# Performance work log

Hardware: AMD Instinct MI355X
Metric: run time of the kernel (lower is better)

Reference implementation:

```python
import jax, jax.numpy as jnp
import numpy as np

N = 50000
H = 8
D = 32
E = 400000
IN = 128
NEG_SLOPE = 0.2


def _gat(h, edges, W, al, ar, b):
    # DGL GATConv: fc -> per-head attention logits -> edge softmax over dst -> aggregate
    src, dst = edges[0], edges[1]
    feat = (h @ W).reshape(N, H, D)                      # [N,H,D]
    el = jnp.einsum('nhd,hd->nh', feat, al)              # [N,H]
    er = jnp.einsum('nhd,hd->nh', feat, ar)              # [N,H]
    e = jax.nn.leaky_relu(el[src] + er[dst], NEG_SLOPE)  # [E,H]
    m = jax.ops.segment_max(e, dst, num_segments=N)      # [N,H] per-dst max
    m = jnp.where(jnp.isfinite(m), m, 0.0)
    m = jax.lax.stop_gradient(m)
    ex = jnp.exp(e - m[dst])                             # [E,H]
    denom = jax.ops.segment_sum(ex, dst, num_segments=N) # [N,H]
    alpha = ex / denom[dst]                              # edge softmax
    out = jax.ops.segment_sum(feat[src] * alpha[:, :, None], dst, num_segments=N)  # [N,H,D]
    return (out + b.reshape(1, H, D)).reshape(N, H * D)


def setup_inputs() -> dict:
    key = jax.random.key(0)
    ks = jax.random.split(key, 12)
    s = 0.05
    return {
        'h': jax.random.normal(ks[0], (N, IN), jnp.float32),
        'edges0': jax.random.randint(ks[1], (2, E), 0, N, jnp.int32),
        'edges1': jax.random.randint(ks[2], (2, E), 0, N, jnp.int32),
        'fc0': jax.random.normal(ks[3], (IN, H * D), jnp.float32) * s,
        'al0': jax.random.normal(ks[4], (H, D), jnp.float32) * s,
        'ar0': jax.random.normal(ks[5], (H, D), jnp.float32) * s,
        'bias0': jnp.zeros((H * D,), jnp.float32),
        'fc1': jax.random.normal(ks[6], (IN, H * D), jnp.float32) * s,
        'al1': jax.random.normal(ks[7], (H, D), jnp.float32) * s,
        'ar1': jax.random.normal(ks[8], (H, D), jnp.float32) * s,
        'bias1': jnp.zeros((H * D,), jnp.float32),
        'sw1': jax.random.normal(ks[9], (H * D, 128), jnp.float32) * s,
        'sb1': jnp.zeros((128,), jnp.float32),
        'sw2': jax.random.normal(ks[10], (128, 1), jnp.float32) * s,
    }


def reference(h, edges0, edges1, fc0, al0, ar0, bias0, fc1, al1, ar1, bias1, sw1, sb1, sw2):
    z0 = _gat(h, edges0, fc0, al0, ar0, bias0)   # [N, H*D]
    z1 = _gat(h, edges1, fc1, al1, ar1, bias1)   # [N, H*D]
    z = jnp.stack([z0, z1], axis=1)              # [N, M=2, H*D]
    # semantic attention: MLP -> mean over nodes -> softmax over meta-paths
    w = jnp.tanh(z @ sw1 + sb1) @ sw2            # [N,M,1]
    beta = jax.nn.softmax(w.mean(axis=0), axis=0)  # [M,1]
    return (beta[None] * z).sum(axis=1)          # [N, H*D]
```

## Files before the change

kernel.cpp:

```cpp
#include <hip/hip_runtime.h>
#include <math.h>

#define NEG_SLOPE 0.2f

typedef unsigned int uint;
typedef unsigned short ushort;
typedef __bf16 bf16x8 __attribute__((ext_vector_type(8)));
typedef float f32x4 __attribute__((ext_vector_type(4)));

__device__ __forceinline__ uint bf16r(float a) {
    uint u = __float_as_uint(a);
    return (u + 0x7fffu + ((u >> 16) & 1u)) >> 16;
}
__device__ __forceinline__ uint bf16pack(float a, float b) {
    return bf16r(a) | (bf16r(b) << 16);
}
__device__ __forceinline__ float bflo(uint u) { return __uint_as_float(u << 16); }
__device__ __forceinline__ float bfhi(uint u) { return __uint_as_float(u & 0xffff0000u); }

__device__ __forceinline__ float fast_tanh(float x) {
    x = fminf(fmaxf(x, -15.f), 15.f);
    float t = __expf(2.f * x);
    return 1.f - 2.f * __builtin_amdgcn_rcpf(t + 1.f);
}

__global__ void prep_kernel(const float* __restrict__ fc0, const float* __restrict__ fc1,
                            const float* __restrict__ sw1, ushort* __restrict__ wbt,
                            ushort* __restrict__ sw1t, float* __restrict__ wsum,
                            int* __restrict__ gcur,
                            int* __restrict__ count, int* __restrict__ cursor, int Ntot) {
    int b = blockIdx.x;
    if (b == 0 && threadIdx.x == 0) { wsum[0] = 0.f; wsum[1] = 0.f; }
    if (b == 0 && threadIdx.x == 1) { *gcur = 0; }
    if (b < 256) {
        int idx = b * 256 + threadIdx.x;
        const float* W = (idx >> 15) ? fc1 : fc0;
        int r = idx & 32767;
        int c = r >> 7, k = r & 127;
        wbt[idx] = (ushort)bf16r(W[(size_t)k * 256 + c]);
    } else if (b < 384) {
        int idx = (b - 256) * 256 + threadIdx.x;
        int c = idx >> 8, p = idx & 255;
        int col = (p & ~63) + ((p & 3) * 16) + ((p >> 2) & 15);
        sw1t[idx] = (ushort)bf16r(sw1[(size_t)col * 128 + c]);
    } else {
        int i = (b - 384) * 256 + threadIdx.x;
        if (i < Ntot) { count[i] = 0; cursor[i] = 0; }
    }
}

__global__ void hist_kernel(const int* __restrict__ e0, const int* __restrict__ e1,
                            int* __restrict__ count, int E, int N) {
    int e = blockIdx.x * blockDim.x + threadIdx.x;
    if (e >= 2 * E) return;
    int l = (e >= E);
    int ee = e - l * E;
    const int* edges = l ? e1 : e0;
    atomicAdd(&count[edges[E + ee] + l * N], 1);
}

__global__ void alloc_kernel(const int* __restrict__ count, int* __restrict__ row0,
                             int* __restrict__ gcur, int Ntot) {
    int i = blockIdx.x * 256 + threadIdx.x;
    int v = (i < Ntot) ? count[i] : 0;
    int lane = threadIdx.x & 63;
    int x = v;
#pragma unroll
    for (int s = 1; s < 64; s <<= 1) {
        int y = __shfl_up(x, s, 64);
        if (lane >= s) x += y;
    }
    int wtot = __shfl(x, 63, 64);
    int wbase = 0;
    if (lane == 0) wbase = atomicAdd(gcur, wtot);
    wbase = __shfl(wbase, 0, 64);
    if (i < Ntot) row0[i] = wbase + x - v;
}

#define HKPAD 136
__global__ void __launch_bounds__(256, 4)
fc_kernel(const float* __restrict__ h, const ushort* __restrict__ wbt,
          const float* __restrict__ al0, const float* __restrict__ ar0,
          const float* __restrict__ al1, const float* __restrict__ ar1,
          ushort* __restrict__ featb, float* __restrict__ el,
          float* __restrict__ er, int N, int nb) {
    __shared__ ushort hs[64 * HKPAD];
    int b = blockIdx.x;
    int l = (b >= nb);
    int n0 = (b - l * nb) * 64;
    for (int t = threadIdx.x; t < 64 * 32; t += 256) {
        int r = t >> 5, i4 = t & 31;
        int n = n0 + r;
        float4 v = make_float4(0.f, 0.f, 0.f, 0.f);
        if (n < N) v = ((const float4*)h)[(size_t)n * 32 + i4];
        uint2 pk;
        pk.x = bf16pack(v.x, v.y);
        pk.y = bf16pack(v.z, v.w);
        *((uint2*)(hs + r * HKPAD + i4 * 4)) = pk;
    }
    __syncthreads();

    const ushort* wb = wbt + l * 32768;
    const float* al = l ? al1 : al0;
    const float* ar = l ? ar1 : ar0;
    ushort* fb = featb + (size_t)l * N * 256;
    float* elp = el + (size_t)l * N * 8;
    float* erp = er + (size_t)l * N * 8;

    int wv = threadIdx.x >> 6;
    int lane = threadIdx.x & 63;
    int lhi = lane >> 4, llo = lane & 15;

    f32x4 acc[4][4];
#pragma unroll
    for (int cb = 0; cb < 4; cb++)
#pragma unroll
        for (int rt = 0; rt < 4; rt++) acc[cb][rt] = (f32x4){0.f, 0.f, 0.f, 0.f};

#pragma unroll
    for (int ks = 0; ks < 4; ks++) {
        bf16x8 a[4];
#pragma unroll
        for (int rt = 0; rt < 4; rt++)
            a[rt] = *(const bf16x8*)(hs + (rt * 16 + llo) * HKPAD + ks * 32 + lhi * 8);
#pragma unroll
        for (int cb = 0; cb < 4; cb++) {
            bf16x8 bfrag = *(const bf16x8*)(wb + (size_t)(64 * wv + 16 * cb + llo) * 128 + ks * 32 + lhi * 8);
#pragma unroll
            for (int rt = 0; rt < 4; rt++)
                acc[cb][rt] = __builtin_amdgcn_mfma_f32_16x16x32_bf16(a[rt], bfrag, acc[cb][rt], 0, 0, 0);
        }
    }

    float alv0 = al[64 * wv + llo],      alv1 = al[64 * wv + 16 + llo];
    float alv2 = al[64 * wv + 32 + llo], alv3 = al[64 * wv + 48 + llo];
    float arv0 = ar[64 * wv + llo],      arv1 = ar[64 * wv + 16 + llo];
    float arv2 = ar[64 * wv + 32 + llo], arv3 = ar[64 * wv + 48 + llo];

#pragma unroll
    for (int rt = 0; rt < 4; rt++) {
#pragma unroll
        for (int reg = 0; reg < 4; reg++) {
            int n = n0 + rt * 16 + lhi * 4 + reg;
            bool valid = (n < N);
            uint2 pv;
            pv.x = bf16pack(acc[0][rt][reg], acc[1][rt][reg]);
            pv.y = bf16pack(acc[2][rt][reg], acc[3][rt][reg]);
            if (valid) *((uint2*)(fb + (size_t)n * 256 + 64 * wv + 4 * llo)) = pv;
            float pl0 = acc[0][rt][reg] * alv0 + acc[1][rt][reg] * alv1;
            float pl1 = acc[2][rt][reg] * alv2 + acc[3][rt][reg] * alv3;
            float pr0 = acc[0][rt][reg] * arv0 + acc[1][rt][reg] * arv1;
            float pr1 = acc[2][rt][reg] * arv2 + acc[3][rt][reg] * arv3;
#pragma unroll
            for (int s = 1; s <= 8; s <<= 1) {
                pl0 += __shfl_xor(pl0, s, 64);
                pl1 += __shfl_xor(pl1, s, 64);
                pr0 += __shfl_xor(pr0, s, 64);
                pr1 += __shfl_xor(pr1, s, 64);
            }
            if (llo == 0 && valid) {
                *((float2*)(elp + (size_t)n * 8 + 2 * wv)) = make_float2(pl0, pl1);
                *((float2*)(erp + (size_t)n * 8 + 2 * wv)) = make_float2(pr0, pr1);
            }
        }
    }
}

__global__ void scatter_kernel(const int* __restrict__ e0, const int* __restrict__ e1,
                               const float* __restrict__ el, const float* __restrict__ er,
                               const int* __restrict__ row0, int* __restrict__ cursor,
                               int* __restrict__ csr_src, float* __restrict__ pedge,
                               int E, int N) {
    int e = blockIdx.x * blockDim.x + threadIdx.x;
    if (e >= 2 * E) return;
    int l = (e >= E);
    int ee = e - l * E;
    const int* edges = l ? e1 : e0;
    int src = edges[ee];
    int dst = edges[E + ee];
    int d = dst + l * N;
    int pos = row0[d] + atomicAdd(&cursor[d], 1);
    csr_src[pos] = src;
    size_t so = (size_t)(l * N + src) * 2;
    size_t dofs = (size_t)(l * N + dst) * 2;
    float4 l0 = ((const float4*)el)[so];
    float4 l1 = ((const float4*)el)[so + 1];
    float4 r0 = ((const float4*)er)[dofs];
    float4 r1 = ((const float4*)er)[dofs + 1];
    float v[8] = {l0.x + r0.x, l0.y + r0.y, l0.z + r0.z, l0.w + r0.w,
                  l1.x + r1.x, l1.y + r1.y, l1.z + r1.z, l1.w + r1.w};
#pragma unroll
    for (int k = 0; k < 8; k++) {
        float t = (v[k] > 0.f) ? v[k] : NEG_SLOPE * v[k];
        v[k] = __expf(t);
    }
    ((float4*)pedge)[pos * 2]     = make_float4(v[0], v[1], v[2], v[3]);
    ((float4*)pedge)[pos * 2 + 1] = make_float4(v[4], v[5], v[6], v[7]);
}

__global__ void aggregate_csr_kernel(const int* __restrict__ csr_src, const float* __restrict__ pedge,
                                     const int* __restrict__ row0arr, const int* __restrict__ count,
                                     const ushort* __restrict__ featb,
                                     const float* __restrict__ bias0, const float* __restrict__ bias1,
                                     ushort* __restrict__ z0b, ushort* __restrict__ z1b, int N) {
    int wid = threadIdx.x >> 6;
    int lane = threadIdx.x & 63;
    int d = blockIdx.x * 4 + wid;
    if (d >= 2 * N) return;
    int l = (d >= N);
    int dst = d - l * N;
    int row0 = row0arr[d];
    int deg = count[d];
    int w = lane >> 4, llo = lane & 15;
    const float2* pe = (const float2*)(pedge + (size_t)row0 * 8);
    const int* cs = csr_src + row0;
    const uint2* fb2 = (const uint2*)(featb + (size_t)l * N * 256);

    float d0 = 0.f, d1 = 0.f;
    float4 a = make_float4(0.f, 0.f, 0.f, 0.f);
    int t = 0;
    for (; t + 4 <= deg; t += 4) {
        int s0 = cs[t], s1 = cs[t + 1], s2 = cs[t + 2], s3 = cs[t + 3];
        float2 q0 = pe[t * 4 + w];
        float2 q1 = pe[t * 4 + 4 + w];
        float2 q2 = pe[t * 4 + 8 + w];
        float2 q3 = pe[t * 4 + 12 + w];
        uint2 u0 = fb2[(size_t)s0 * 64 + lane];
        uint2 u1 = fb2[(size_t)s1 * 64 + lane];
        uint2 u2 = fb2[(size_t)s2 * 64 + lane];
        uint2 u3 = fb2[(size_t)s3 * 64 + lane];
        d0 += q0.x; d1 += q0.y;
        a.x += q0.x * bflo(u0.x); a.y += q0.x * bfhi(u0.x);
        a.z += q0.y * bflo(u0.y); a.w += q0.y * bfhi(u0.y);
        d0 += q1.x; d1 += q1.y;
        a.x += q1.x * bflo(u1.x); a.y += q1.x * bfhi(u1.x);
        a.z += q1.y * bflo(u1.y); a.w += q1.y * bfhi(u1.y);
        d0 += q2.x; d1 += q2.y;
        a.x += q2.x * bflo(u2.x); a.y += q2.x * bfhi(u2.x);
        a.z += q2.y * bflo(u2.y); a.w += q2.y * bfhi(u2.y);
        d0 += q3.x; d1 += q3.y;
        a.x += q3.x * bflo(u3.x); a.y += q3.x * bfhi(u3.x);
        a.z += q3.y * bflo(u3.y); a.w += q3.y * bfhi(u3.y);
    }
    for (; t < deg; t++) {
        int s0 = cs[t];
        float2 q0 = pe[t * 4 + w];
        uint2 u0 = fb2[(size_t)s0 * 64 + lane];
        d0 += q0.x; d1 += q0.y;
        a.x += q0.x * bflo(u0.x); a.y += q0.x * bfhi(u0.x);
        a.z += q0.y * bflo(u0.y); a.w += q0.y * bfhi(u0.y);
    }
    const float* bias = l ? bias1 : bias0;
    int c0 = 64 * w + llo;
    float b0 = bias[c0], b1 = bias[c0 + 16], b2 = bias[c0 + 32], b3 = bias[c0 + 48];
    float i0 = (d0 > 0.f) ? 1.f / d0 : 0.f;
    float i1 = (d1 > 0.f) ? 1.f / d1 : 0.f;
    uint2 o;
    o.x = bf16pack(a.x * i0 + b0, a.y * i0 + b1);
    o.y = bf16pack(a.z * i1 + b2, a.w * i1 + b3);
    ushort* zb = l ? z1b : z0b;
    ((uint2*)zb)[(size_t)dst * 64 + lane] = o;
}

#define ZROW 264
__global__ void __launch_bounds__(256, 4)
semantic_kernel(const ushort* __restrict__ z0b, const ushort* __restrict__ z1b,
                const ushort* __restrict__ sw1t, const float* __restrict__ sb1,
                const float* __restrict__ sw2, float* __restrict__ wsum, int N) {
    __shared__ ushort zs[64 * ZROW];
    __shared__ float rowp[64];
    int n0 = blockIdx.x * 32;
    if (threadIdx.x < 64) rowp[threadIdx.x] = 0.f;
    for (int t = threadIdx.x; t < 64 * 32; t += 256) {
        int row = t >> 5, i16 = t & 31;
        int r = row >> 1, mm = row & 1;
        int n = n0 + r;
        uint4 v = make_uint4(0u, 0u, 0u, 0u);
        if (n < N) v = ((const uint4*)(mm ? z1b : z0b))[(size_t)n * 32 + i16];
        *((uint4*)(zs + row * ZROW + i16 * 8)) = v;
    }
    __syncthreads();

    int wv = threadIdx.x >> 6;
    int lane = threadIdx.x & 63;
    int lhi = lane >> 4, llo = lane & 15;

    f32x4 acc[2][4];
#pragma unroll
    for (int c = 0; c < 2; c++)
#pragma unroll
        for (int rt = 0; rt < 4; rt++) acc[c][rt] = (f32x4){0.f, 0.f, 0.f, 0.f};

#pragma unroll
    for (int ks = 0; ks < 8; ks++) {
        bf16x8 b0 = *(const bf16x8*)(sw1t + (size_t)((2 * wv) * 16 + llo) * 256 + ks * 32 + lhi * 8);
        bf16x8 b1 = *(const bf16x8*)(sw1t + (size_t)((2 * wv + 1) * 16 + llo) * 256 + ks * 32 + lhi * 8);
#pragma unroll
        for (int rt = 0; rt < 4; rt++) {
            bf16x8 av = *(const bf16x8*)(zs + (rt * 16 + llo) * ZROW + ks * 32 + lhi * 8);
            acc[0][rt] = __builtin_amdgcn_mfma_f32_16x16x32_bf16(av, b0, acc[0][rt], 0, 0, 0);
            acc[1][rt] = __builtin_amdgcn_mfma_f32_16x16x32_bf16(av, b1, acc[1][rt], 0, 0, 0);
        }
    }

    float sb0 = sb1[(2 * wv) * 16 + llo],      s20 = sw2[(2 * wv) * 16 + llo];
    float sb1v = sb1[(2 * wv + 1) * 16 + llo], s21 = sw2[(2 * wv + 1) * 16 + llo];
#pragma unroll
    for (int rt = 0; rt < 4; rt++) {
        float pr[4];
#pragma unroll
        for (int reg = 0; reg < 4; reg++)
            pr[reg] = fast_tanh(acc[0][rt][reg] + sb0) * s20 + fast_tanh(acc[1][rt][reg] + sb1v) * s21;
#pragma unroll
        for (int s = 1; s <= 8; s <<= 1)
#pragma unroll
            for (int reg = 0; reg < 4; reg++) pr[reg] += __shfl_xor(pr[reg], s, 64);
        if (llo == 0) {
#pragma unroll
            for (int reg = 0; reg < 4; reg++)
                atomicAdd(&rowp[rt * 16 + lhi * 4 + reg], pr[reg]);
        }
    }
    __syncthreads();
    if (threadIdx.x < 64) {
        int node = n0 + (threadIdx.x >> 1);
        float v = (node < N) ? rowp[threadIdx.x] : 0.f;
        v += __shfl_xor(v, 2, 64);
        v += __shfl_xor(v, 4, 64);
        v += __shfl_xor(v, 8, 64);
        v += __shfl_xor(v, 16, 64);
        v += __shfl_xor(v, 32, 64);
        if (threadIdx.x < 2) atomicAdd(&wsum[threadIdx.x], v);
    }
}

__global__ void combine_kernel(float* __restrict__ out, const ushort* __restrict__ z0b,
                               const ushort* __restrict__ z1b, const float* __restrict__ wsum,
                               float invN, int N) {
    int idx = blockIdx.x * 256 + threadIdx.x;
    if (idx >= N * 64) return;
    float w0 = wsum[0] * invN, w1 = wsum[1] * invN;
    float mx = fmaxf(w0, w1);
    float e0 = __expf(w0 - mx), e1 = __expf(w1 - mx);
    float b0 = e0 / (e0 + e1), b1 = e1 / (e0 + e1);
    int n = idx >> 6, lane = idx & 63;
    int w = lane >> 4, llo = lane & 15;
    uint2 a = ((const uint2*)z0b)[idx];
    uint2 b = ((const uint2*)z1b)[idx];
    float* o = out + (size_t)n * 256 + 64 * w + llo;
    o[0]  = b0 * bflo(a.x) + b1 * bflo(b.x);
    o[16] = b0 * bfhi(a.x) + b1 * bfhi(b.x);
    o[32] = b0 * bflo(a.y) + b1 * bflo(b.y);
    o[48] = b0 * bfhi(a.y) + b1 * bfhi(b.y);
}

extern "C" void kernel_launch(void* const* d_in, const int* in_sizes, int n_in,
                              void* d_out, int out_size, void* d_ws, size_t ws_size,
                              hipStream_t stream) {
    const float* h      = (const float*)d_in[0];
    const int*   edges0 = (const int*)d_in[1];
    const int*   edges1 = (const int*)d_in[2];
    const float* fc0    = (const float*)d_in[3];
    const float* al0    = (const float*)d_in[4];
    const float* ar0    = (const float*)d_in[5];
    const float* bias0  = (const float*)d_in[6];
    const float* fc1    = (const float*)d_in[7];
    const float* al1    = (const float*)d_in[8];
    const float* ar1    = (const float*)d_in[9];
    const float* bias1  = (const float*)d_in[10];
    const float* sw1    = (const float*)d_in[11];
    const float* sb1    = (const float*)d_in[12];
    const float* sw2    = (const float*)d_in[13];

    const int N = in_sizes[0] / 128;
    const int E = in_sizes[1] / 2;
    const int Ntot = 2 * N;
    const int NB2 = (Ntot + 255) / 256;
    const int nb = (N + 63) / 64;

    char* ws = (char*)d_ws;
    ushort* featb = (ushort*)ws;
    ushort* z0b   = featb + (size_t)Ntot * 256;
    ushort* z1b   = z0b + (size_t)N * 256;
    ushort* wbt   = z1b + (size_t)N * 256;
    ushort* sw1t  = wbt + 2 * 256 * 128;
    float*  el    = (float*)(sw1t + 128 * 256);
    float*  er    = el + (size_t)Ntot * 8;
    float*  pedge = er + (size_t)Ntot * 8;
    int*    csr_src = (int*)(pedge + (size_t)E * 16);
    int*    count   = csr_src + 2 * E;
    int*    row0    = count + Ntot;
    int*    cursor  = row0 + Ntot;
    int*    gcur    = cursor + Ntot;
    float*  wsum  = (float*)(gcur + 1);
    float*  outp  = (float*)d_out;

    prep_kernel<<<384 + NB2, 256, 0, stream>>>(fc0, fc1, sw1, wbt, sw1t, wsum, gcur,
                                               count, cursor, Ntot);
    hist_kernel<<<(2 * E + 255) / 256, 256, 0, stream>>>(edges0, edges1, count, E, N);
    alloc_kernel<<<NB2, 256, 0, stream>>>(count, row0, gcur, Ntot);
    fc_kernel<<<2 * nb, 256, 0, stream>>>(h, wbt, al0, ar0, al1, ar1, featb, el, er, N, nb);
    scatter_kernel<<<(2 * E + 255) / 256, 256, 0, stream>>>(edges0, edges1, el, er, row0,
                                                            cursor, csr_src, pedge, E, N);
    aggregate_csr_kernel<<<(Ntot + 3) / 4, 256, 0, stream>>>(csr_src, pedge, row0, count,
                                                             featb, bias0, bias1, z0b, z1b, N);
    semantic_kernel<<<(N + 31) / 32, 256, 0, stream>>>(z0b, z1b, sw1t, sb1, sw2, wsum, N);
    combine_kernel<<<(N * 64 + 255) / 256, 256, 0, stream>>>(outp, z0b, z1b, wsum,
                                                             1.0f / (float)N, N);
}
```

Before: 270.6 us.

## Fuse histogram into prep, scan into fc, store edge weights as bf16

The edge-destination histogram moves into the weight-prep kernel and the CSR offset scan moves into extra blocks of the fc kernel. Count and cursor are now zeroed with a single memset, which removes two kernel launches and their serialization points. Per-edge softmax numerators are stored as packed bf16 instead of fp32, halving scatter writes and aggregate reads. The cost is reduced precision on the attention weights and denominators.

```diff
diff --git a/kernel.cpp b/kernel.cpp
--- a/kernel.cpp
+++ b/kernel.cpp
@@ -24,11 +24,12 @@
     return 1.f - 2.f * __builtin_amdgcn_rcpf(t + 1.f);
 }
 
-__global__ void prep_kernel(const float* __restrict__ fc0, const float* __restrict__ fc1,
-                            const float* __restrict__ sw1, ushort* __restrict__ wbt,
-                            ushort* __restrict__ sw1t, float* __restrict__ wsum,
-                            int* __restrict__ gcur,
-                            int* __restrict__ count, int* __restrict__ cursor, int Ntot) {
+__global__ void prep_hist_kernel(const float* __restrict__ fc0, const float* __restrict__ fc1,
+                                 const float* __restrict__ sw1, ushort* __restrict__ wbt,
+                                 ushort* __restrict__ sw1t, float* __restrict__ wsum,
+                                 int* __restrict__ gcur,
+                                 const int* __restrict__ e0, const int* __restrict__ e1,
+                                 int* __restrict__ count, int E, int N) {
     int b = blockIdx.x;
     if (b == 0 && threadIdx.x == 0) { wsum[0] = 0.f; wsum[1] = 0.f; }
     if (b == 0 && threadIdx.x == 1) { *gcur = 0; }
@@ -44,48 +45,44 @@
         int col = (p & ~63) + ((p & 3) * 16) + ((p >> 2) & 15);
         sw1t[idx] = (ushort)bf16r(sw1[(size_t)col * 128 + c]);
     } else {
-        int i = (b - 384) * 256 + threadIdx.x;
-        if (i < Ntot) { count[i] = 0; cursor[i] = 0; }
-    }
-}
-
-__global__ void hist_kernel(const int* __restrict__ e0, const int* __restrict__ e1,
-                            int* __restrict__ count, int E, int N) {
-    int e = blockIdx.x * blockDim.x + threadIdx.x;
-    if (e >= 2 * E) return;
-    int l = (e >= E);
-    int ee = e - l * E;
-    const int* edges = l ? e1 : e0;
-    atomicAdd(&count[edges[E + ee] + l * N], 1);
-}
-
-__global__ void alloc_kernel(const int* __restrict__ count, int* __restrict__ row0,
-                             int* __restrict__ gcur, int Ntot) {
-    int i = blockIdx.x * 256 + threadIdx.x;
-    int v = (i < Ntot) ? count[i] : 0;
-    int lane = threadIdx.x & 63;
-    int x = v;
-#pragma unroll
-    for (int s = 1; s < 64; s <<= 1) {
-        int y = __shfl_up(x, s, 64);
-        if (lane >= s) x += y;
-    }
-    int wtot = __shfl(x, 63, 64);
-    int wbase = 0;
-    if (lane == 0) wbase = atomicAdd(gcur, wtot);
-    wbase = __shfl(wbase, 0, 64);
-    if (i < Ntot) row0[i] = wbase + x - v;
+        int e = (b - 384) * 256 + threadIdx.x;
+        if (e < 2 * E) {
+            int l = (e >= E);
+            int ee = e - l * E;
+            const int* edges = l ? e1 : e0;
+            atomicAdd(&count[edges[E + ee] + l * N], 1);
+        }
+    }
 }
 
 #define HKPAD 136
 __global__ void __launch_bounds__(256, 4)
-fc_kernel(const float* __restrict__ h, const ushort* __restrict__ wbt,
-          const float* __restrict__ al0, const float* __restrict__ ar0,
-          const float* __restrict__ al1, const float* __restrict__ ar1,
-          ushort* __restrict__ featb, float* __restrict__ el,
-          float* __restrict__ er, int N, int nb) {
+fc_alloc_kernel(const float* __restrict__ h, const ushort* __restrict__ wbt,
+                const float* __restrict__ al0, const float* __restrict__ ar0,
+                const float* __restrict__ al1, const float* __restrict__ ar1,
+                ushort* __restrict__ featb, float* __restrict__ el,
+                float* __restrict__ er, int N, int nb,
+                const int* __restrict__ count, int* __restrict__ row0_out,
+                int* __restrict__ gcur, int Ntot) {
     __shared__ ushort hs[64 * HKPAD];
     int b = blockIdx.x;
+    if (b >= 2 * nb) {
+        int i = (b - 2 * nb) * 256 + threadIdx.x;
+        int v = (i < Ntot) ? count[i] : 0;
+        int lane = threadIdx.x & 63;
+        int x = v;
+#pragma unroll
+        for (int s = 1; s < 64; s <<= 1) {
+            int y = __shfl_up(x, s, 64);
+            if (lane >= s) x += y;
+        }
+        int wtot = __shfl(x, 63, 64);
+        int wbase = 0;
+        if (lane == 0) wbase = atomicAdd(gcur, wtot);
+        wbase = __shfl(wbase, 0, 64);
+        if (i < Ntot) row0_out[i] = wbase + x - v;
+        return;
+    }
     int l = (b >= nb);
     int n0 = (b - l * nb) * 64;
     for (int t = threadIdx.x; t < 64 * 32; t += 256) {
@@ -169,7 +166,7 @@
 __global__ void scatter_kernel(const int* __restrict__ e0, const int* __restrict__ e1,
                                const float* __restrict__ el, const float* __restrict__ er,
                                const int* __restrict__ row0, int* __restrict__ cursor,
-                               int* __restrict__ csr_src, float* __restrict__ pedge,
+                               int* __restrict__ csr_src, ushort* __restrict__ pedgeb,
                                int E, int N) {
     int e = blockIdx.x * blockDim.x + threadIdx.x;
     if (e >= 2 * E) return;
@@ -194,11 +191,21 @@
         float t = (v[k] > 0.f) ? v[k] : NEG_SLOPE * v[k];
         v[k] = __expf(t);
     }
-    ((float4*)pedge)[pos * 2]     = make_float4(v[0], v[1], v[2], v[3]);
-    ((float4*)pedge)[pos * 2 + 1] = make_float4(v[4], v[5], v[6], v[7]);
-}
-
-__global__ void aggregate_csr_kernel(const int* __restrict__ csr_src, const float* __restrict__ pedge,
+    uint4 pk;
+    pk.x = bf16pack(v[0], v[1]);
+    pk.y = bf16pack(v[2], v[3]);
+    pk.z = bf16pack(v[4], v[5]);
+    pk.w = bf16pack(v[6], v[7]);
+    ((uint4*)pedgeb)[pos] = pk;
+}
+
+#define AGG_STEP(qq, uu) {                                      \
+    float qx = bflo(qq), qy = bfhi(qq);                         \
+    d0 += qx; d1 += qy;                                         \
+    a.x += qx * bflo((uu).x); a.y += qx * bfhi((uu).x);         \
+    a.z += qy * bflo((uu).y); a.w += qy * bfhi((uu).y); }
+
+__global__ void aggregate_csr_kernel(const int* __restrict__ csr_src, const ushort* __restrict__ pedgeb,
                                      const int* __restrict__ row0arr, const int* __restrict__ count,
                                      const ushort* __restrict__ featb,
                                      const float* __restrict__ bias0, const float* __restrict__ bias1,
@@ -212,7 +219,7 @@
     int row0 = row0arr[d];
     int deg = count[d];
     int w = lane >> 4, llo = lane & 15;
-    const float2* pe = (const float2*)(pedge + (size_t)row0 * 8);
+    const uint* peu = (const uint*)pedgeb + (size_t)row0 * 4;
     const int* cs = csr_src + row0;
     const uint2* fb2 = (const uint2*)(featb + (size_t)l * N * 256);
 
@@ -221,34 +228,24 @@
     int t = 0;
     for (; t + 4 <= deg; t += 4) {
         int s0 = cs[t], s1 = cs[t + 1], s2 = cs[t + 2], s3 = cs[t + 3];
-        float2 q0 = pe[t * 4 + w];
-        float2 q1 = pe[t * 4 + 4 + w];
-        float2 q2 = pe[t * 4 + 8 + w];
-        float2 q3 = pe[t * 4 + 12 + w];
+        uint q0 = peu[t * 4 + w];
+        uint q1 = peu[t * 4 + 4 + w];
+        uint q2 = peu[t * 4 + 8 + w];
+        uint q3 = peu[t * 4 + 12 + w];
         uint2 u0 = fb2[(size_t)s0 * 64 + lane];
         uint2 u1 = fb2[(size_t)s1 * 64 + lane];
         uint2 u2 = fb2[(size_t)s2 * 64 + lane];
         uint2 u3 = fb2[(size_t)s3 * 64 + lane];
-        d0 += q0.x; d1 += q0.y;
-        a.x += q0.x * bflo(u0.x); a.y += q0.x * bfhi(u0.x);
-        a.z += q0.y * bflo(u0.y); a.w += q0.y * bfhi(u0.y);
-        d0 += q1.x; d1 += q1.y;
-        a.x += q1.x * bflo(u1.x); a.y += q1.x * bfhi(u1.x);
-        a.z += q1.y * bflo(u1.y); a.w += q1.y * bfhi(u1.y);
-        d0 += q2.x; d1 += q2.y;
-        a.x += q2.x * bflo(u2.x); a.y += q2.x * bfhi(u2.x);
-        a.z += q2.y * bflo(u2.y); a.w += q2.y * bfhi(u2.y);
-        d0 += q3.x; d1 += q3.y;
-        a.x += q3.x * bflo(u3.x); a.y += q3.x * bfhi(u3.x);
-        a.z += q3.y * bflo(u3.y); a.w += q3.y * bfhi(u3.y);
+        AGG_STEP(q0, u0)
+        AGG_STEP(q1, u1)
+        AGG_STEP(q2, u2)
+        AGG_STEP(q3, u3)
     }
     for (; t < deg; t++) {
         int s0 = cs[t];
-        float2 q0 = pe[t * 4 + w];
+        uint q0 = peu[t * 4 + w];
         uint2 u0 = fb2[(size_t)s0 * 64 + lane];
-        d0 += q0.x; d1 += q0.y;
-        a.x += q0.x * bflo(u0.x); a.y += q0.x * bfhi(u0.x);
-        a.z += q0.y * bflo(u0.y); a.w += q0.y * bfhi(u0.y);
+        AGG_STEP(q0, u0)
     }
     const float* bias = l ? bias1 : bias0;
     int c0 = 64 * w + llo;
@@ -377,32 +374,34 @@
     const int Ntot = 2 * N;
     const int NB2 = (Ntot + 255) / 256;
     const int nb = (N + 63) / 64;
+    const int nbE = (2 * E + 255) / 256;
 
     char* ws = (char*)d_ws;
-    ushort* featb = (ushort*)ws;
-    ushort* z0b   = featb + (size_t)Ntot * 256;
-    ushort* z1b   = z0b + (size_t)N * 256;
-    ushort* wbt   = z1b + (size_t)N * 256;
-    ushort* sw1t  = wbt + 2 * 256 * 128;
-    float*  el    = (float*)(sw1t + 128 * 256);
-    float*  er    = el + (size_t)Ntot * 8;
-    float*  pedge = er + (size_t)Ntot * 8;
-    int*    csr_src = (int*)(pedge + (size_t)E * 16);
+    ushort* featb  = (ushort*)ws;
+    ushort* z0b    = featb + (size_t)Ntot * 256;
+    ushort* z1b    = z0b + (size_t)N * 256;
+    ushort* wbt    = z1b + (size_t)N * 256;
+    ushort* sw1t   = wbt + 2 * 256 * 128;
+    float*  el     = (float*)(sw1t + 128 * 256);
+    float*  er     = el + (size_t)Ntot * 8;
+    ushort* pedgeb = (ushort*)(er + (size_t)Ntot * 8);
+    int*    csr_src = (int*)(pedgeb + (size_t)E * 16);
     int*    count   = csr_src + 2 * E;
-    int*    row0    = count + Ntot;
-    int*    cursor  = row0 + Ntot;
-    int*    gcur    = cursor + Ntot;
+    int*    cursor  = count + Ntot;
+    int*    row0    = cursor + Ntot;
+    int*    gcur    = row0 + Ntot;
     float*  wsum  = (float*)(gcur + 1);
     float*  outp  = (float*)d_out;
 
-    prep_kernel<<<384 + NB2, 256, 0, stream>>>(fc0, fc1, sw1, wbt, sw1t, wsum, gcur,
-                                               count, cursor, Ntot);
-    hist_kernel<<<(2 * E + 255) / 256, 256, 0, stream>>>(edges0, edges1, count, E, N);
-    alloc_kernel<<<NB2, 256, 0, stream>>>(count, row0, gcur, Ntot);
-    fc_kernel<<<2 * nb, 256, 0, stream>>>(h, wbt, al0, ar0, al1, ar1, featb, el, er, N, nb);
-    scatter_kernel<<<(2 * E + 255) / 256, 256, 0, stream>>>(edges0, edges1, el, er, row0,
-                                                            cursor, csr_src, pedge, E, N);
-    aggregate_csr_kernel<<<(Ntot + 3) / 4, 256, 0, stream>>>(csr_src, pedge, row0, count,
+    hipMemsetAsync(count, 0, sizeof(int) * 2 * (size_t)Ntot, stream);
+    prep_hist_kernel<<<384 + nbE, 256, 0, stream>>>(fc0, fc1, sw1, wbt, sw1t, wsum, gcur,
+                                                    edges0, edges1, count, E, N);
+    fc_alloc_kernel<<<2 * nb + NB2, 256, 0, stream>>>(h, wbt, al0, ar0, al1, ar1,
+                                                      featb, el, er, N, nb,
+                                                      count, row0, gcur, Ntot);
+    scatter_kernel<<<nbE, 256, 0, stream>>>(edges0, edges1, el, er, row0,
+                                            cursor, csr_src, pedgeb, E, N);
+    aggregate_csr_kernel<<<(Ntot + 3) / 4, 256, 0, stream>>>(csr_src, pedgeb, row0, count,
                                                              featb, bias0, bias1, z0b, z1b, N);
     semantic_kernel<<<(N + 31) / 32, 256, 0, stream>>>(z0b, z1b, sw1t, sb1, sw2, wsum, N);
     combine_kernel<<<(N * 64 + 255) / 256, 256, 0, stream>>>(outp, z0b, z1b, wsum,
```

New measurement: 262.8 us. 2.9% less time.
